# Performance work log

Hardware: AMD Instinct MI355X
Metric: run time of the kernel (lower is better)

## Reference

```python
import jax, jax.numpy as jnp
import numpy as np

B, S, D, H = 1, 2048, 768, 12
WIN = 128            # window_size
HALF = WIN // 2      # 64
WN = WIN + 1         # each position attends to [i-64, i+64] inclusive -> 129 keys
DH = D // H


def setup_inputs() -> dict:
    key = jax.random.key(0)
    ks = jax.random.split(key, 8)
    scale = 0.02
    return {
        "query": jax.random.normal(ks[0], (B, S, D), dtype=jnp.float32),
        "key":   jax.random.normal(ks[1], (B, S, D), dtype=jnp.float32),
        "value": jax.random.normal(ks[2], (B, S, D), dtype=jnp.float32),
        "Wq": jax.random.normal(ks[3], (D, D), dtype=jnp.float32) * scale,
        "bq": jnp.zeros((D,), dtype=jnp.float32),
        "Wk": jax.random.normal(ks[4], (D, D), dtype=jnp.float32) * scale,
        "bk": jnp.zeros((D,), dtype=jnp.float32),
        "Wv": jax.random.normal(ks[5], (D, D), dtype=jnp.float32) * scale,
        "bv": jnp.zeros((D,), dtype=jnp.float32),
        "Wo": jax.random.normal(ks[6], (D, D), dtype=jnp.float32) * scale,
        "bo": jnp.zeros((D,), dtype=jnp.float32),
    }


def reference(query, key, value, Wq, bq, Wk, bk, Wv, bv, Wo, bo):
    b, s, d = query.shape
    # Linear projections, split heads: [B,S,H,DH]
    q = (query @ Wq + bq).reshape(b, s, H, DH)
    k = (key   @ Wk + bk).reshape(b, s, H, DH)
    v = (value @ Wv + bv).reshape(b, s, H, DH)

    # Window gather indices: pos[i, j] = i - HALF + j, j in [0, WN)
    pos = jnp.arange(s)[:, None] + (jnp.arange(WN)[None, :] - HALF)  # [S, WN]
    valid = (pos >= 0) & (pos < s)                                   # [S, WN]
    idx = jnp.clip(pos, 0, s - 1)

    kw = k[:, idx]  # [B, S, WN, H, DH]
    vw = v[:, idx]  # [B, S, WN, H, DH]

    scores = jnp.einsum('bshd,bswhd->bhsw', q, kw) / np.sqrt(DH)     # [B,H,S,WN]
    scores = jnp.where(valid[None, None, :, :], scores, -jnp.inf)
    attn = jax.nn.softmax(scores, axis=-1)

    ctx = jnp.einsum('bhsw,bswhd->bshd', attn, vw).reshape(b, s, d)  # [B,S,D]
    return ctx @ Wo + bo
```

## Files before the change

kernel.cpp:

```cpp
#include <hip/hip_runtime.h>
#include <math.h>

#define S_LEN 2048
#define DM 768
#define NHEAD 12
#define DHEAD 64
#define HALF_W 64

typedef _Float16 half8 __attribute__((ext_vector_type(8)));
typedef _Float16 half4_t __attribute__((ext_vector_type(4)));
typedef float floatx4 __attribute__((ext_vector_type(4)));

typedef const __attribute__((address_space(1))) unsigned int* gas_ptr;
typedef __attribute__((address_space(3))) unsigned int* las_ptr;
__device__ __forceinline__ void gld_lds16(const void* g, void* l) {
  __builtin_amdgcn_global_load_lds((gas_ptr)g, (las_ptr)l, 16, 0, 0);
}

__global__ __launch_bounds__(256)
void prep_w_kernel(const float* __restrict__ Wq, const float* __restrict__ Wk,
                   const float* __restrict__ Wv, const float* __restrict__ Wo,
                   _Float16* __restrict__ Tq, _Float16* __restrict__ Tk,
                   _Float16* __restrict__ Tv, _Float16* __restrict__ To) {
  __shared__ float t[64][65];
  int b = blockIdx.x;
  int z = b / 144, rem = b % 144;
  const float* W = z == 0 ? Wq : z == 1 ? Wk : z == 2 ? Wv : Wo;
  _Float16* T = z == 0 ? Tq : z == 1 ? Tk : z == 2 ? Tv : To;
  int n0 = (rem % 12) * 64, k0 = (rem / 12) * 64;
  int tx = threadIdx.x & 15, ty = threadIdx.x >> 4;
#pragma unroll
  for (int i = 0; i < 4; ++i) {
    int row = ty + i * 16;
    float4 v = *(const float4*)(W + (size_t)(k0 + row) * DM + n0 + tx * 4);
    t[row][tx * 4 + 0] = v.x; t[row][tx * 4 + 1] = v.y;
    t[row][tx * 4 + 2] = v.z; t[row][tx * 4 + 3] = v.w;
  }
  __syncthreads();
#pragma unroll
  for (int i = 0; i < 4; ++i) {
    int nn = ty + i * 16, kk = tx * 4;
    half4_t h = {(_Float16)t[kk + 0][nn], (_Float16)t[kk + 1][nn],
                 (_Float16)t[kk + 2][nn], (_Float16)t[kk + 3][nn]};
    *(half4_t*)(T + (size_t)(n0 + nn) * DM + k0 + kk) = h;
  }
}

#define GBM 64
#define GBN 64
#define GBK 64

__global__ __launch_bounds__(256, 6)
void gemm_qkv_kernel(const float* __restrict__ A0, const float* __restrict__ A1,
                     const float* __restrict__ A2, const _Float16* __restrict__ W0,
                     const _Float16* __restrict__ W1, const _Float16* __restrict__ W2,
                     const float* __restrict__ b0, const float* __restrict__ b1,
                     const float* __restrict__ b2, _Float16* __restrict__ Q,
                     _Float16* __restrict__ K, _Float16* __restrict__ Vt) {
  __shared__ __align__(16) float Asf[GBM * GBK];
  __shared__ __align__(16) _Float16 Bs[GBN * GBK];
  const int z = blockIdx.z;
  const float* A = z == 0 ? A0 : z == 1 ? A1 : A2;
  const _Float16* Wt = z == 0 ? W0 : z == 1 ? W1 : W2;
  const float* bias = z == 0 ? b0 : z == 1 ? b1 : b2;

  const int tid = threadIdx.x;
  const int lane = tid & 63;
  const int w = tid >> 6;
  const int lr = lane & 15;
  const int lq = lane >> 4;
  const int wm = w >> 1, wn = w & 1;
  const int m0 = blockIdx.y * GBM;
  const int n0 = blockIdx.x * GBN;
  const int wb = tid & 192;

  floatx4 acc[2][2] = {};

  for (int k0 = 0; k0 < DM; k0 += GBK) {
    __syncthreads();
#pragma unroll
    for (int i = 0; i < 4; ++i) {
      int c = i * 256 + tid;
      int m = c >> 4, j = c & 15, jg = j ^ (m & 14);
      gld_lds16(A + (size_t)(m0 + m) * DM + k0 + jg * 4, &Asf[(i * 256 + wb) * 4]);
    }
#pragma unroll
    for (int i = 0; i < 2; ++i) {
      int c = i * 256 + tid;
      int n = c >> 3, j = c & 7, jg = j ^ (n & 7);
      gld_lds16(Wt + (size_t)(n0 + n) * DM + k0 + jg * 8, &Bs[(i * 256 + wb) * 8]);
    }
    __syncthreads();

#pragma unroll
    for (int kh = 0; kh < 2; ++kh) {
      half8 af[2], bf[2];
#pragma unroll
      for (int mt = 0; mt < 2; ++mt) {
        int m = wm * 32 + mt * 16 + lr;
        int j0 = (kh * 8 + lq * 2) ^ (m & 14);
        float4 f0 = *(const float4*)&Asf[(m * 16 + j0) * 4];
        float4 f1 = *(const float4*)&Asf[(m * 16 + j0 + 1) * 4];
        af[mt] = half8{(_Float16)f0.x, (_Float16)f0.y, (_Float16)f0.z, (_Float16)f0.w,
                       (_Float16)f1.x, (_Float16)f1.y, (_Float16)f1.z, (_Float16)f1.w};
      }
#pragma unroll
      for (int nt = 0; nt < 2; ++nt) {
        int n = wn * 32 + nt * 16 + lr;
        int j = (kh * 4 + lq) ^ (n & 7);
        bf[nt] = *(const half8*)&Bs[n * GBK + j * 8];
      }
#pragma unroll
      for (int mt = 0; mt < 2; ++mt)
#pragma unroll
        for (int nt = 0; nt < 2; ++nt)
          acc[mt][nt] = __builtin_amdgcn_mfma_f32_16x16x32_f16(af[mt], bf[nt], acc[mt][nt], 0, 0, 0);
    }
  }

#pragma unroll
  for (int mt = 0; mt < 2; ++mt) {
    int row0 = m0 + wm * 32 + mt * 16 + lq * 4;
#pragma unroll
    for (int nt = 0; nt < 2; ++nt) {
      int col = n0 + wn * 32 + nt * 16 + lr;
      float bv = bias[col];
      if (z == 2) {
        half4_t o = {(_Float16)(acc[mt][nt][0] + bv), (_Float16)(acc[mt][nt][1] + bv),
                     (_Float16)(acc[mt][nt][2] + bv), (_Float16)(acc[mt][nt][3] + bv)};
        *(half4_t*)(Vt + (size_t)col * S_LEN + row0) = o;
      } else {
        _Float16* H = z == 0 ? Q : K;
#pragma unroll
        for (int rr = 0; rr < 4; ++rr)
          H[(size_t)(row0 + rr) * DM + col] = (_Float16)(acc[mt][nt][rr] + bv);
      }
    }
  }
}

__global__ __launch_bounds__(256, 6)
void gemm_out_kernel(const _Float16* __restrict__ A, const _Float16* __restrict__ Wt,
                     const float* __restrict__ bias, float* __restrict__ C) {
  __shared__ __align__(16) _Float16 As[GBM * GBK];
  __shared__ __align__(16) _Float16 Bs[GBN * GBK];
  const int tid = threadIdx.x;
  const int lane = tid & 63;
  const int w = tid >> 6;
  const int lr = lane & 15;
  const int lq = lane >> 4;
  const int wm = w >> 1, wn = w & 1;
  const int m0 = blockIdx.y * GBM;
  const int n0 = blockIdx.x * GBN;
  const int wb = tid & 192;

  floatx4 acc[2][2] = {};

  for (int k0 = 0; k0 < DM; k0 += GBK) {
    __syncthreads();
#pragma unroll
    for (int i = 0; i < 2; ++i) {
      int c = i * 256 + tid;
      int m = c >> 3, j = c & 7, jg = j ^ (m & 7);
      gld_lds16(A + (size_t)(m0 + m) * DM + k0 + jg * 8, &As[(i * 256 + wb) * 8]);
    }
#pragma unroll
    for (int i = 0; i < 2; ++i) {
      int c = i * 256 + tid;
      int n = c >> 3, j = c & 7, jg = j ^ (n & 7);
      gld_lds16(Wt + (size_t)(n0 + n) * DM + k0 + jg * 8, &Bs[(i * 256 + wb) * 8]);
    }
    __syncthreads();

#pragma unroll
    for (int kh = 0; kh < 2; ++kh) {
      half8 af[2], bf[2];
#pragma unroll
      for (int mt = 0; mt < 2; ++mt) {
        int m = wm * 32 + mt * 16 + lr;
        int j = (kh * 4 + lq) ^ (m & 7);
        af[mt] = *(const half8*)&As[m * GBK + j * 8];
      }
#pragma unroll
      for (int nt = 0; nt < 2; ++nt) {
        int n = wn * 32 + nt * 16 + lr;
        int j = (kh * 4 + lq) ^ (n & 7);
        bf[nt] = *(const half8*)&Bs[n * GBK + j * 8];
      }
#pragma unroll
      for (int mt = 0; mt < 2; ++mt)
#pragma unroll
        for (int nt = 0; nt < 2; ++nt)
          acc[mt][nt] = __builtin_amdgcn_mfma_f32_16x16x32_f16(af[mt], bf[nt], acc[mt][nt], 0, 0, 0);
    }
  }

#pragma unroll
  for (int mt = 0; mt < 2; ++mt) {
    int row0 = m0 + wm * 32 + mt * 16 + lq * 4;
#pragma unroll
    for (int nt = 0; nt < 2; ++nt) {
      int col = n0 + wn * 32 + nt * 16 + lr;
      float bv = bias[col];
#pragma unroll
      for (int rr = 0; rr < 4; ++rr)
        C[(size_t)(row0 + rr) * DM + col] = acc[mt][nt][rr] + bv;
    }
  }
}

#define ATQ 32

__global__ __launch_bounds__(256, 3)
void swattn_mfma_kernel(const _Float16* __restrict__ qh, const _Float16* __restrict__ kh,
                        const _Float16* __restrict__ vt, _Float16* __restrict__ ctx) {
  __shared__ __align__(16) _Float16 Ks[160 * 64];
  __shared__ __align__(16) _Float16 Vs[64 * 168];
  __shared__ __align__(16) _Float16 QP[32 * 168];
  __shared__ float red[4][32];

  const int tid = threadIdx.x;
  const int lane = tid & 63, w = tid >> 6;
  const int lr = lane & 15, lq = lane >> 4;
  const int bid = blockIdx.x;
  const int x = bid & 7, mid = (bid >> 3) & 7, h = bid >> 6;
  const int s0 = (x * 8 + mid) * ATQ;
  const int wb = tid & 192;

  {
    int r = tid >> 3, j = tid & 7, jg = j ^ (r & 7);
    gld_lds16(qh + (size_t)(s0 + r) * DM + h * DHEAD + jg * 8, &QP[wb * 8]);
  }
#pragma unroll
  for (int i = 0; i < 5; ++i) {
    int c = i * 256 + tid;
    int r = c >> 3, j = c & 7, jg = j ^ (r & 7);
    int pos = s0 - HALF_W + r;
    pos = pos < 0 ? 0 : (pos > S_LEN - 1 ? S_LEN - 1 : pos);
    gld_lds16(kh + (size_t)pos * DM + h * DHEAD + jg * 8, &Ks[(i * 256 + wb) * 8]);
  }
#pragma unroll
  for (int i = 0; i < 6; ++i) {
    int c = i * 256 + tid;
    if (c < 1344) {
      int r = c / 21, j = c % 21;
      int cb = s0 - HALF_W + j * 8;
      cb = cb < 0 ? 0 : (cb > S_LEN - 8 ? S_LEN - 8 : cb);
      gld_lds16(vt + (size_t)(h * DHEAD + r) * S_LEN + cb, &Vs[(i * 256 + wb) * 8]);
    }
  }
  __syncthreads();

  const int qt = w & 1, ph = w >> 1;
  floatx4 sc[5];
  {
    half8 aq[2];
#pragma unroll
    for (int k2 = 0; k2 < 2; ++k2) {
      int r = qt * 16 + lr, j = (k2 * 4 + lq) ^ (r & 7);
      aq[k2] = *(const half8*)&QP[r * DHEAD + j * 8];
    }
#pragma unroll
    for (int t = 0; t < 5; ++t) {
      int pt = ph * 5 + t;
      floatx4 a = {};
#pragma unroll
      for (int k2 = 0; k2 < 2; ++k2) {
        int r = pt * 16 + lr, j = (k2 * 4 + lq) ^ (r & 7);
        half8 bk = *(const half8*)&Ks[r * DHEAD + j * 8];
        a = __builtin_amdgcn_mfma_f32_16x16x32_f16(aq[k2], bk, a, 0, 0, 0);
      }
      sc[t] = a;
    }
  }

  const int qbase = qt * 16 + lq * 4;
  float m4[4] = {-1e30f, -1e30f, -1e30f, -1e30f};
#pragma unroll
  for (int t = 0; t < 5; ++t) {
    int p = (ph * 5 + t) * 16 + lr;
    int g = s0 - HALF_W + p;
#pragma unroll
    for (int rr = 0; rr < 4; ++rr) {
      int q = qbase + rr;
      bool ok = (p >= q) && (p <= q + 128) && (g >= 0) && (g < S_LEN);
      float v = ok ? sc[t][rr] * 0.125f : -1e30f;
      sc[t][rr] = v;
      m4[rr] = fmaxf(m4[rr], v);
    }
  }
#pragma unroll
  for (int off = 1; off <= 8; off <<= 1)
#pragma unroll
    for (int rr = 0; rr < 4; ++rr) m4[rr] = fmaxf(m4[rr], __shfl_xor(m4[rr], off, 64));
  if (lr == 0)
#pragma unroll
    for (int rr = 0; rr < 4; ++rr) red[ph][qbase + rr] = m4[rr];
  __syncthreads();

  float ss[4] = {0.f, 0.f, 0.f, 0.f};
  float mm[4];
#pragma unroll
  for (int rr = 0; rr < 4; ++rr)
    mm[rr] = fmaxf(red[0][qbase + rr], red[1][qbase + rr]);
#pragma unroll
  for (int t = 0; t < 5; ++t)
#pragma unroll
    for (int rr = 0; rr < 4; ++rr) {
      float e = __expf(sc[t][rr] - mm[rr]);
      sc[t][rr] = e;
      ss[rr] += e;
    }
#pragma unroll
  for (int off = 1; off <= 8; off <<= 1)
#pragma unroll
    for (int rr = 0; rr < 4; ++rr) ss[rr] += __shfl_xor(ss[rr], off, 64);
  if (lr == 0)
#pragma unroll
    for (int rr = 0; rr < 4; ++rr) red[2 + ph][qbase + rr] = ss[rr];
  __syncthreads();

#pragma unroll
  for (int rr = 0; rr < 4; ++rr) {
    float inv = 1.f / (red[2][qbase + rr] + red[3][qbase + rr]);
#pragma unroll
    for (int t = 0; t < 5; ++t) {
      int p = (ph * 5 + t) * 16 + lr;
      QP[(qbase + rr) * 168 + p] = (_Float16)(sc[t][rr] * inv);
    }
  }
  __syncthreads();

  {
    const int qt2 = w & 1;
    const int dt0 = (w >> 1) * 2;
    floatx4 a0 = {}, a1 = {};
#pragma unroll
    for (int ks = 0; ks < 5; ++ks) {
      half8 ap = *(const half8*)&QP[(qt2 * 16 + lr) * 168 + ks * 32 + lq * 8];
      half8 bv0 = *(const half8*)&Vs[(dt0 * 16 + lr) * 168 + ks * 32 + lq * 8];
      half8 bv1 = *(const half8*)&Vs[((dt0 + 1) * 16 + lr) * 168 + ks * 32 + lq * 8];
      a0 = __builtin_amdgcn_mfma_f32_16x16x32_f16(ap, bv0, a0, 0, 0, 0);
      a1 = __builtin_amdgcn_mfma_f32_16x16x32_f16(ap, bv1, a1, 0, 0, 0);
    }
#pragma unroll
    for (int rr = 0; rr < 4; ++rr) {
      size_t row = (size_t)(s0 + qt2 * 16 + lq * 4 + rr) * DM + h * DHEAD;
      ctx[row + dt0 * 16 + lr] = (_Float16)a0[rr];
      ctx[row + (dt0 + 1) * 16 + lr] = (_Float16)a1[rr];
    }
  }
}

extern "C" void kernel_launch(void* const* d_in, const int* in_sizes, int n_in,
                              void* d_out, int out_size, void* d_ws, size_t ws_size,
                              hipStream_t stream) {
  const float* query = (const float*)d_in[0];
  const float* key   = (const float*)d_in[1];
  const float* value = (const float*)d_in[2];
  const float* Wq = (const float*)d_in[3];
  const float* bq = (const float*)d_in[4];
  const float* Wk = (const float*)d_in[5];
  const float* bk = (const float*)d_in[6];
  const float* Wv = (const float*)d_in[7];
  const float* bv = (const float*)d_in[8];
  const float* Wo = (const float*)d_in[9];
  const float* bo = (const float*)d_in[10];
  float* out = (float*)d_out;

  const size_t nel = (size_t)S_LEN * DM;
  const size_t wel = (size_t)DM * DM;
  _Float16* Wtq = (_Float16*)d_ws;
  _Float16* Wtk = Wtq + wel;
  _Float16* Wtv = Wtk + wel;
  _Float16* Wto = Wtv + wel;
  _Float16* qh = Wto + wel;
  _Float16* khb = qh + nel;
  _Float16* Vtg = khb + nel;
  _Float16* ctxh = Vtg + nel;

  prep_w_kernel<<<dim3(576), 256, 0, stream>>>(Wq, Wk, Wv, Wo, Wtq, Wtk, Wtv, Wto);
  gemm_qkv_kernel<<<dim3(DM / GBN, S_LEN / GBM, 3), 256, 0, stream>>>(
      query, key, value, Wtq, Wtk, Wtv, bq, bk, bv, qh, khb, Vtg);
  swattn_mfma_kernel<<<dim3((S_LEN / ATQ) * NHEAD), 256, 0, stream>>>(qh, khb, Vtg, ctxh);
  gemm_out_kernel<<<dim3(DM / GBN, S_LEN / GBM), 256, 0, stream>>>(ctxh, Wto, bo, out);
}
```

Measured before the change: 149.9 us.

## Remap GEMM blocks to XCD-local panels and pad A tile instead of swizzle

Both GEMMs switch to a 1D grid whose block index is remapped so that blocks sharing an A row panel land on the same XCD, which should improve L2 reuse of the fp32 activations across the chiplets. The QKV kernel also replaces the XOR swizzle of the fp32 A tile in LDS with a padded layout of 17 chunks per row, filled by a fifth partial load pass. The padding costs extra LDS and an extra load instruction per k-step, and may change bank-conflict behaviour.

```diff
diff --git a/kernel.cpp b/kernel.cpp
--- a/kernel.cpp
+++ b/kernel.cpp
@@ -49,6 +49,7 @@
 #define GBM 64
 #define GBN 64
 #define GBK 64
+#define ACH 17
 
 __global__ __launch_bounds__(256, 6)
 void gemm_qkv_kernel(const float* __restrict__ A0, const float* __restrict__ A1,
@@ -57,9 +58,16 @@
                      const float* __restrict__ b0, const float* __restrict__ b1,
                      const float* __restrict__ b2, _Float16* __restrict__ Q,
                      _Float16* __restrict__ K, _Float16* __restrict__ Vt) {
-  __shared__ __align__(16) float Asf[GBM * GBK];
+  __shared__ __align__(16) float Asf[GBM * ACH * 4];
   __shared__ __align__(16) _Float16 Bs[GBN * GBK];
-  const int z = blockIdx.z;
+  const int bid = blockIdx.x;
+  const int xcd = bid & 7;
+  const int li = bid >> 3;
+  const int panel = xcd * 12 + li / 12;
+  const int nb = li % 12;
+  const int z = panel >> 5;
+  const int m0 = (panel & 31) * GBM;
+  const int n0 = nb * GBN;
   const float* A = z == 0 ? A0 : z == 1 ? A1 : A2;
   const _Float16* Wt = z == 0 ? W0 : z == 1 ? W1 : W2;
   const float* bias = z == 0 ? b0 : z == 1 ? b1 : b2;
@@ -70,8 +78,6 @@
   const int lr = lane & 15;
   const int lq = lane >> 4;
   const int wm = w >> 1, wn = w & 1;
-  const int m0 = blockIdx.y * GBM;
-  const int n0 = blockIdx.x * GBN;
   const int wb = tid & 192;
 
   floatx4 acc[2][2] = {};
@@ -79,10 +85,13 @@
   for (int k0 = 0; k0 < DM; k0 += GBK) {
     __syncthreads();
 #pragma unroll
-    for (int i = 0; i < 4; ++i) {
-      int c = i * 256 + tid;
-      int m = c >> 4, j = c & 15, jg = j ^ (m & 14);
-      gld_lds16(A + (size_t)(m0 + m) * DM + k0 + jg * 4, &Asf[(i * 256 + wb) * 4]);
+    for (int i = 0; i < 5; ++i) {
+      if (i < 4 || tid < 64) {
+        int s = i * 256 + tid;
+        int m = s / ACH, pos = s % ACH;
+        int ch = pos < 16 ? pos : 15;
+        gld_lds16(A + (size_t)(m0 + m) * DM + k0 + ch * 4, &Asf[(i * 256 + wb) * 4]);
+      }
     }
 #pragma unroll
     for (int i = 0; i < 2; ++i) {
@@ -98,9 +107,9 @@
 #pragma unroll
       for (int mt = 0; mt < 2; ++mt) {
         int m = wm * 32 + mt * 16 + lr;
-        int j0 = (kh * 8 + lq * 2) ^ (m & 14);
-        float4 f0 = *(const float4*)&Asf[(m * 16 + j0) * 4];
-        float4 f1 = *(const float4*)&Asf[(m * 16 + j0 + 1) * 4];
+        int j0 = kh * 8 + lq * 2;
+        float4 f0 = *(const float4*)&Asf[(m * ACH + j0) * 4];
+        float4 f1 = *(const float4*)&Asf[(m * ACH + j0 + 1) * 4];
         af[mt] = half8{(_Float16)f0.x, (_Float16)f0.y, (_Float16)f0.z, (_Float16)f0.w,
                        (_Float16)f1.x, (_Float16)f1.y, (_Float16)f1.z, (_Float16)f1.w};
       }
@@ -144,14 +153,17 @@
                      const float* __restrict__ bias, float* __restrict__ C) {
   __shared__ __align__(16) _Float16 As[GBM * GBK];
   __shared__ __align__(16) _Float16 Bs[GBN * GBK];
+  const int bid = blockIdx.x;
+  const int xcd = bid & 7;
+  const int li = bid >> 3;
+  const int m0 = (xcd * 4 + li / 12) * GBM;
+  const int n0 = (li % 12) * GBN;
   const int tid = threadIdx.x;
   const int lane = tid & 63;
   const int w = tid >> 6;
   const int lr = lane & 15;
   const int lq = lane >> 4;
   const int wm = w >> 1, wn = w & 1;
-  const int m0 = blockIdx.y * GBM;
-  const int n0 = blockIdx.x * GBN;
   const int wb = tid & 192;
 
   floatx4 acc[2][2] = {};
@@ -380,8 +392,8 @@
   _Float16* ctxh = Vtg + nel;
 
   prep_w_kernel<<<dim3(576), 256, 0, stream>>>(Wq, Wk, Wv, Wo, Wtq, Wtk, Wtv, Wto);
-  gemm_qkv_kernel<<<dim3(DM / GBN, S_LEN / GBM, 3), 256, 0, stream>>>(
+  gemm_qkv_kernel<<<dim3(1152), 256, 0, stream>>>(
       query, key, value, Wtq, Wtk, Wtv, bq, bk, bv, qh, khb, Vtg);
   swattn_mfma_kernel<<<dim3((S_LEN / ATQ) * NHEAD), 256, 0, stream>>>(qh, khb, Vtg, ctxh);
-  gemm_out_kernel<<<dim3(DM / GBN, S_LEN / GBM), 256, 0, stream>>>(ctxh, Wto, bo, out);
-}
+  gemm_out_kernel<<<dim3(384), 256, 0, stream>>>(ctxh, Wto, bo, out);
+}
```

New measurement: 135.4 us. 9.7% less time.
